# Kernel optimization log

Measured on AMD Instinct MI355X. Metric: run time of the kernel, lower is better.

The kernel has to match this reference:

```python
import jax, jax.numpy as jnp
import numpy as np
from jax import lax

BLOCK_SIZE = 7
DROP_PROB = 0.1


def setup_inputs() -> dict:
    key = jax.random.key(0)
    kx, ku = jax.random.split(key)
    N, C, H, W = 64, 256, 64, 64
    x = jax.random.normal(kx, (N, C, H, W), dtype=jnp.float32)
    # one uniform draw per valid top-left block position, shared over N and C
    u = jax.random.uniform(ku, (H - BLOCK_SIZE + 1, W - BLOCK_SIZE + 1), dtype=jnp.float32)
    return {"x": x, "u": u}


def _block_mask(u, h, w):
    # drop[i,j] = 1 -> block with top-left (i,j) is dropped
    drop = (u < DROP_PROB).astype(jnp.float32)  # [h-bs+1, w-bs+1]
    # dilate: a pixel (y,x) is zeroed if ANY block covering it was dropped.
    # max-pool with window=bs, stride=1, pad=bs-1 on both sides -> [h, w]
    pad = BLOCK_SIZE - 1
    dilated = lax.reduce_window(
        drop, 0.0, lax.max,
        window_dimensions=(BLOCK_SIZE, BLOCK_SIZE),
        window_strides=(1, 1),
        padding=((pad, pad), (pad, pad)),
    )
    return 1.0 - dilated  # [h, w], 1 = keep


def reference(x, u):
    _, _, h, w = x.shape
    mask = _block_mask(u, h, w)                       # [h, w]
    scale = (h * w) / mask.sum()                      # numel/sum ratio (N,C cancel)
    return x * (mask * scale)[None, None, :, :]
```

## Files before the change

kernel.cpp:

```cpp
#include <hip/hip_runtime.h>

#define BS 7
#define DROPP 0.1f
#define UH 58
#define UW 58

typedef float f32x4 __attribute__((ext_vector_type(4)));

__global__ __launch_bounds__(1024) void dropblock_mask_kernel(
    const float* __restrict__ u, float* __restrict__ m)
{
    __shared__ unsigned long long sD[64];
    __shared__ unsigned long long sR[64];
    __shared__ unsigned long long sDil[64];
    __shared__ float sscale;

    const int tid  = threadIdx.x;
    const int wave = tid >> 6;
    const int lane = tid & 63;

    for (int i = wave; i < 64; i += 16) {
        bool d = false;
        if (i < UH && lane < UW) d = (u[i * UW + lane] < DROPP);
        unsigned long long D = __ballot(d);
        if (lane == 0) sD[i] = D;
    }
    __syncthreads();

    if (wave == 0) {
        unsigned long long D = sD[lane];
        unsigned long long R = D;
        #pragma unroll
        for (int s = 1; s <= 6; ++s) R |= (D << s);
        sR[lane] = R;
    }
    __syncthreads();

    if (wave == 0) {
        const int y = lane;
        const int i0 = (y - 6 > 0) ? (y - 6) : 0;
        const int i1 = (y < UH - 1) ? y : (UH - 1);
        unsigned long long dil = 0ull;
        for (int i = i0; i <= i1; ++i) dil |= sR[i];
        sDil[y] = dil;
        float kept = (float)(64 - __popcll(dil));
        #pragma unroll
        for (int off = 32; off >= 1; off >>= 1)
            kept += __shfl_down(kept, off, 64);
        if (lane == 0) sscale = 4096.0f / kept;
    }
    __syncthreads();

    const float s = sscale;
    const unsigned long long dil = sDil[(tid >> 4) & 63];
    const int xb = (tid * 4) & 63;
    f32x4 mv;
    mv.x = ((dil >> (xb + 0)) & 1ull) ? 0.0f : s;
    mv.y = ((dil >> (xb + 1)) & 1ull) ? 0.0f : s;
    mv.z = ((dil >> (xb + 2)) & 1ull) ? 0.0f : s;
    mv.w = ((dil >> (xb + 3)) & 1ull) ? 0.0f : s;
    ((f32x4*)m)[tid] = mv;
}

__global__ __launch_bounds__(256) void dropblock_apply_kernel(
    const f32x4* __restrict__ x, const f32x4* __restrict__ m4,
    f32x4* __restrict__ out)
{
    const int gid = blockIdx.x * 256 + threadIdx.x;
    const f32x4 xv = __builtin_nontemporal_load(&x[gid]);
    const f32x4 mv = m4[gid & 1023];
    f32x4 ov = xv * mv;
    __builtin_nontemporal_store(ov, &out[gid]);
}

extern "C" void kernel_launch(void* const* d_in, const int* in_sizes, int n_in,
                              void* d_out, int out_size, void* d_ws, size_t ws_size,
                              hipStream_t stream) {
    const float* x = (const float*)d_in[0];
    const float* u = (const float*)d_in[1];
    float* out = (float*)d_out;
    float* m   = (float*)d_ws;

    dropblock_mask_kernel<<<1, 1024, 0, stream>>>(u, m);

    const int total4 = out_size / 4;
    dropblock_apply_kernel<<<total4 / 256, 256, 0, stream>>>(
        (const f32x4*)x, (const f32x4*)m, (f32x4*)out);
}
```

Before: 417.5 us.

## Skip loading input for fully dropped pixel groups using bitmask in apply kernel

The mask kernel now writes only the 64 dilated row bitmasks and the scale to workspace, instead of a full float mask. The apply kernel processes 8 elements per thread and decodes mask bits inline. When all 8 pixels in a group are dropped it skips loading x and writes zeros, cutting read traffic when the dilated mask covers much of the image. The branch and per-lane mask decode add some ALU work and possible divergence.

Result: no change. 414.7 us (-0.7%).

```diff
diff --git a/kernel.cpp b/kernel.cpp
--- a/kernel.cpp
+++ b/kernel.cpp
@@ -8,12 +8,10 @@
 typedef float f32x4 __attribute__((ext_vector_type(4)));
 
 __global__ __launch_bounds__(1024) void dropblock_mask_kernel(
-    const float* __restrict__ u, float* __restrict__ m)
+    const float* __restrict__ u, unsigned long long* __restrict__ dws)
 {
     __shared__ unsigned long long sD[64];
     __shared__ unsigned long long sR[64];
-    __shared__ unsigned long long sDil[64];
-    __shared__ float sscale;
 
     const int tid  = threadIdx.x;
     const int wave = tid >> 6;
@@ -42,35 +40,47 @@
         const int i1 = (y < UH - 1) ? y : (UH - 1);
         unsigned long long dil = 0ull;
         for (int i = i0; i <= i1; ++i) dil |= sR[i];
-        sDil[y] = dil;
+        dws[y] = dil;
         float kept = (float)(64 - __popcll(dil));
         #pragma unroll
         for (int off = 32; off >= 1; off >>= 1)
             kept += __shfl_down(kept, off, 64);
-        if (lane == 0) sscale = 4096.0f / kept;
+        if (lane == 0) ((float*)(dws + 64))[0] = 4096.0f / kept;
     }
-    __syncthreads();
-
-    const float s = sscale;
-    const unsigned long long dil = sDil[(tid >> 4) & 63];
-    const int xb = (tid * 4) & 63;
-    f32x4 mv;
-    mv.x = ((dil >> (xb + 0)) & 1ull) ? 0.0f : s;
-    mv.y = ((dil >> (xb + 1)) & 1ull) ? 0.0f : s;
-    mv.z = ((dil >> (xb + 2)) & 1ull) ? 0.0f : s;
-    mv.w = ((dil >> (xb + 3)) & 1ull) ? 0.0f : s;
-    ((f32x4*)m)[tid] = mv;
 }
 
 __global__ __launch_bounds__(256) void dropblock_apply_kernel(
-    const f32x4* __restrict__ x, const f32x4* __restrict__ m4,
+    const f32x4* __restrict__ x, const unsigned long long* __restrict__ dws,
     f32x4* __restrict__ out)
 {
     const int gid = blockIdx.x * 256 + threadIdx.x;
-    const f32x4 xv = __builtin_nontemporal_load(&x[gid]);
-    const f32x4 mv = m4[gid & 1023];
-    f32x4 ov = xv * mv;
-    __builtin_nontemporal_store(ov, &out[gid]);
+    const int g2  = gid * 2;
+    const int y   = (g2 >> 4) & 63;
+    const int xb  = (g2 & 15) * 4;
+
+    const unsigned long long dil = dws[y];
+    const float s = ((const float*)(dws + 64))[0];
+    const unsigned int byt = (unsigned int)((dil >> xb) & 0xFFull);
+
+    f32x4 o0 = {0.0f, 0.0f, 0.0f, 0.0f};
+    f32x4 o1 = o0;
+    if (byt != 0xFFu) {
+        const f32x4 x0 = __builtin_nontemporal_load(&x[g2]);
+        const f32x4 x1 = __builtin_nontemporal_load(&x[g2 + 1]);
+        f32x4 m0, m1;
+        m0.x = (byt &   1u) ? 0.0f : s;
+        m0.y = (byt &   2u) ? 0.0f : s;
+        m0.z = (byt &   4u) ? 0.0f : s;
+        m0.w = (byt &   8u) ? 0.0f : s;
+        m1.x = (byt &  16u) ? 0.0f : s;
+        m1.y = (byt &  32u) ? 0.0f : s;
+        m1.z = (byt &  64u) ? 0.0f : s;
+        m1.w = (byt & 128u) ? 0.0f : s;
+        o0 = x0 * m0;
+        o1 = x1 * m1;
+    }
+    __builtin_nontemporal_store(o0, &out[g2]);
+    __builtin_nontemporal_store(o1, &out[g2 + 1]);
 }
 
 extern "C" void kernel_launch(void* const* d_in, const int* in_sizes, int n_in,
@@ -79,11 +89,12 @@
     const float* x = (const float*)d_in[0];
     const float* u = (const float*)d_in[1];
     float* out = (float*)d_out;
-    float* m   = (float*)d_ws;
+    unsigned long long* dws = (unsigned long long*)d_ws;
 
-    dropblock_mask_kernel<<<1, 1024, 0, stream>>>(u, m);
+    dropblock_mask_kernel<<<1, 1024, 0, stream>>>(u, dws);
 
     const int total4 = out_size / 4;
-    dropblock_apply_kernel<<<total4 / 256, 256, 0, stream>>>(
-        (const f32x4*)x, (const f32x4*)m, (f32x4*)out);
+    const int nthreads = total4 / 2;
+    dropblock_apply_kernel<<<nthreads / 256, 256, 0, stream>>>(
+        (const f32x4*)x, dws, (f32x4*)out);
 }
```
